# Kernel optimization log

Measured on AMD Instinct MI355X. Metric: run time of the kernel, lower is better.

Reference implementation:

```python
import jax, jax.numpy as jnp
import numpy as np

B, H, W = 32, 512, 512

def _sample(img, sx, sy):
    """Bilinear sample img [C,H,W] at source coords sx,sy [H,W]; zeros padding (align_corners=True pixel coords)."""
    C, Hh, Ww = img.shape
    x0 = jnp.floor(sx); y0 = jnp.floor(sy)
    wx = sx - x0; wy = sy - y0
    def gat(xf, yf):
        xi = jnp.clip(xf, 0, Ww - 1).astype(jnp.int32)
        yi = jnp.clip(yf, 0, Hh - 1).astype(jnp.int32)
        valid = ((xf >= 0) & (xf <= Ww - 1) & (yf >= 0) & (yf <= Hh - 1)).astype(img.dtype)
        return img[:, yi, xi] * valid
    return (gat(x0, y0) * (1 - wx) * (1 - wy) + gat(x0 + 1, y0) * wx * (1 - wy)
            + gat(x0, y0 + 1) * (1 - wx) * wy + gat(x0 + 1, y0 + 1) * wx * wy)

def _grid(Hh, Ww, dtype):
    ys, xs = jnp.meshgrid(jnp.arange(Hh, dtype=dtype), jnp.arange(Ww, dtype=dtype), indexing='ij')
    return xs, ys

def _rotate_one(img, angle_deg):
    C, Hh, Ww = img.shape
    th = angle_deg * (jnp.pi / 180.0)
    c, s = jnp.cos(th), jnp.sin(th)
    cx, cy = (Ww - 1) / 2.0, (Hh - 1) / 2.0
    xs, ys = _grid(Hh, Ww, img.dtype)
    dx, dy = xs - cx, ys - cy
    return _sample(img, c * dx + s * dy + cx, -s * dx + c * dy + cy)

def _affine_one(img, tx, ty, sc):
    C, Hh, Ww = img.shape
    cx, cy = (Ww - 1) / 2.0, (Hh - 1) / 2.0
    xs, ys = _grid(Hh, Ww, img.dtype)
    return _sample(img, (xs - cx - tx) / sc + cx, (ys - cy - ty) / sc + cy)

def _rgb_to_hsv(img):
    r, g, b = img[:, 0], img[:, 1], img[:, 2]
    maxc = jnp.maximum(jnp.maximum(r, g), b)
    minc = jnp.minimum(jnp.minimum(r, g), b)
    delta = maxc - minc
    eps = 1e-8
    s = delta / (maxc + eps)
    dd = delta + eps
    rc, gc, bc = (maxc - r) / dd, (maxc - g) / dd, (maxc - b) / dd
    h = jnp.where(maxc == r, bc - gc, jnp.where(maxc == g, 2.0 + rc - bc, 4.0 + gc - rc))
    return (h / 6.0) % 1.0, s, maxc

def _hsv_to_rgb(h, s, v):
    i = jnp.floor(h * 6.0)
    f = h * 6.0 - i
    p, q, t = v * (1 - s), v * (1 - f * s), v * (1 - (1 - f) * s)
    i = i.astype(jnp.int32) % 6
    conds = [i == k for k in range(6)]
    r = jnp.select(conds, [v, q, p, p, t, v])
    g = jnp.select(conds, [t, v, v, q, p, p])
    b = jnp.select(conds, [p, p, t, v, v, q])
    return jnp.stack([r, g, b], axis=1)

def _color_jitter(img, bf, cf, sf, hf):
    bf, cf, sf = (x[:, None, None, None] for x in (bf, cf, sf))
    img = jnp.clip(img * bf, 0.0, 1.0)
    gray = (0.299 * img[:, 0] + 0.587 * img[:, 1] + 0.114 * img[:, 2])[:, None]
    mean = gray.mean(axis=(2, 3), keepdims=True)
    img = jnp.clip(cf * img + (1 - cf) * mean, 0.0, 1.0)
    gray = (0.299 * img[:, 0] + 0.587 * img[:, 1] + 0.114 * img[:, 2])[:, None]
    img = jnp.clip(sf * img + (1 - sf) * gray, 0.0, 1.0)
    h, s, v = _rgb_to_hsv(img)
    h = (h + hf[:, None, None]) % 1.0
    return jnp.clip(_hsv_to_rgb(h, s, v), 0.0, 1.0)

def _forward(imgs, masks, hflip_mask, vflip_mask, angles, translate, scale, brightness, contrast, saturation, hue):
    hm = (hflip_mask > 0)[:, None, None, None]
    vm = (vflip_mask > 0)[:, None, None, None]
    imgs = jnp.where(hm, imgs[..., ::-1], imgs)
    masks = jnp.where(hm, masks[..., ::-1], masks)
    imgs = jnp.where(vm, imgs[..., ::-1, :], imgs)
    masks = jnp.where(vm, masks[..., ::-1, :], masks)
    rot = jax.vmap(_rotate_one)
    imgs = rot(imgs, angles)
    masks = rot(masks, angles)
    tx = translate[:, 0] * W
    ty = translate[:, 1] * H
    aff = jax.vmap(_affine_one)
    imgs = aff(imgs, tx, ty, scale)
    masks = aff(masks, tx, ty, scale)
    imgs = _color_jitter(imgs, brightness, contrast, saturation, hue)
    return imgs, masks

def setup_inputs():
    key = jax.random.key(0)
    ks = jax.random.split(key, 11)
    return {
        "imgs": jax.random.uniform(ks[0], (B, 3, H, W), jnp.float32),
        "masks": (jax.random.uniform(ks[1], (B, 1, H, W)) > 0.5).astype(jnp.float32),
        "hflip_mask": jax.random.randint(ks[2], (B,), 0, 2, jnp.int32),
        "vflip_mask": jax.random.randint(ks[3], (B,), 0, 2, jnp.int32),
        "angles": (jax.random.uniform(ks[4], (B,)) - 0.5) * 180.0,
        "translate": (jax.random.uniform(ks[5], (B, 2)) - 0.5) * 0.2,
        "scale": 0.9 + jax.random.uniform(ks[6], (B,)) * 0.2,
        "brightness": 0.8 + jax.random.uniform(ks[7], (B,)) * 0.4,
        "contrast": 0.8 + jax.random.uniform(ks[8], (B,)) * 0.4,
        "saturation": 0.8 + jax.random.uniform(ks[9], (B,)) * 0.4,
        "hue": (jax.random.uniform(ks[10], (B,)) - 0.5) * 0.2,
    }

def reference(imgs, masks, hflip_mask, vflip_mask, angles, translate, scale, brightness, contrast, saturation, hue):
    return _forward(imgs, masks, hflip_mask, vflip_mask, angles, translate, scale, brightness, contrast, saturation, hue)
```

## Files before the change

### kernel.cpp

```cpp
#include <hip/hip_runtime.h>
#include <hip/hip_fp16.h>
#include <math.h>

#define Wd 512
#define Hd 512
#define Bd 32
#define PLANE (Hd * Wd)

#define WIN 48
#define WSTR 50
#define NPR1 (WIN * (WIN / 2))

#define AWIN 40
#define ASTR 42
#define NPR2 (AWIN * (AWIN / 2))

__device__ __forceinline__ float clip01(float x) { return fminf(fmaxf(x, 0.f), 1.f); }

__device__ __forceinline__ unsigned pack2h(float a, float b) {
    __half2 h = __floats2half2_rn(a, b);
    return *(unsigned*)&h;
}
__device__ __forceinline__ float2 unp2h(unsigned u) {
    return __half22float2(*(__half2*)&u);
}

__global__ __launch_bounds__(256) void k_rotate(const float* __restrict__ imgs,
                                                const float* __restrict__ masks,
                                                const int* __restrict__ hflip,
                                                const int* __restrict__ vflip,
                                                const float* __restrict__ angles,
                                                uint2* __restrict__ rot)
{
    __shared__ uint2 cells[WIN * WSTR];

    const int hw = blockIdx.x;
    const int lt = (hw & 7) * 1024 + (hw >> 3);
    const int b   = lt >> 8;
    const int t   = lt & 255;
    const int bx  = (t & 15) * 32;
    const int by  = (t >> 4) * 32;

    const int tx = threadIdx.x, ty = threadIdx.y;
    const int tid = ty * 32 + tx;

    const float cx = (Wd - 1) * 0.5f, cy = (Hd - 1) * 0.5f;
    const float th = angles[b] * 0.017453292519943295f;
    const float c = cosf(th), s = sinf(th);
    const bool hf = hflip[b] > 0, vf = vflip[b] > 0;

    const float xs0 = (float)bx - cx, xs1 = (float)(bx + 31) - cx;
    const float ys0 = (float)by - cy, ys1 = (float)(by + 31) - cy;
    float a0 = c * xs0 + s * ys0 + cx, a1 = c * xs1 + s * ys0 + cx;
    float a2 = c * xs0 + s * ys1 + cx, a3 = c * xs1 + s * ys1 + cx;
    float b0 = -s * xs0 + c * ys0 + cy, b1 = -s * xs1 + c * ys0 + cy;
    float b2 = -s * xs0 + c * ys1 + cy, b3 = -s * xs1 + c * ys1 + cy;
    float mnx = fminf(fminf(a0, a1), fminf(a2, a3));
    float mxx = fmaxf(fmaxf(a0, a1), fmaxf(a2, a3));
    float mny = fminf(fminf(b0, b1), fminf(b2, b3));
    float mxy = fmaxf(fmaxf(b0, b1), fmaxf(b2, b3));
    const int ox0 = ((int)floorf(hf ? (511.f - mxx) : mnx) - 1) & ~1;
    const int oy0 = (int)floorf(vf ? (511.f - mxy) : mny) - 1;

    const float* ib = imgs + (size_t)b * 3 * PLANE;
    const float* mb = masks + (size_t)b * PLANE;

    #pragma unroll
    for (int it = 0; it < 5; ++it) {
        int slot = tid + it * 256;
        if (it < 4 || slot < NPR1) {
            int row = slot / (WIN / 2);
            int pc  = slot - row * (WIN / 2);
            int gy = min(max(oy0 + row, 0), Hd - 1);
            int gx = min(max(ox0 + 2 * pc, 0), Wd - 2) & ~1;
            int gi = gy * Wd + gx;
            float2 r2 = *(const float2*)(ib + gi);
            float2 g2 = *(const float2*)(ib + gi + PLANE);
            float2 b2v = *(const float2*)(ib + gi + 2 * PLANE);
            float2 m2 = *(const float2*)(mb + gi);
            uint4 w;
            w.x = pack2h(r2.x, g2.x);
            w.y = pack2h(b2v.x, m2.x);
            w.z = pack2h(r2.y, g2.y);
            w.w = pack2h(b2v.y, m2.y);
            *(uint4*)&cells[row * WSTR + 2 * pc] = w;
        }
    }
    __syncthreads();

    #pragma unroll
    for (int k = 0; k < 4; ++k) {
        const int x = bx + tx, y = by + ty + k * 8;
        float dx = (float)x - cx, dy = (float)y - cy;
        float sx = c * dx + s * dy + cx;
        float sy = -s * dx + c * dy + cy;
        if (hf) sx = 511.f - sx;
        if (vf) sy = 511.f - sy;

        float sxl = sx - (float)ox0, syl = sy - (float)oy0;
        float x0f = floorf(sxl), y0f = floorf(syl);
        float wx = sxl - x0f, wy = syl - y0f;
        int xi = min(max((int)x0f, 0), WIN - 2);
        int yi = min(max((int)y0f, 0), WIN - 2);

        float fx0 = (float)ox0 + x0f, fy0 = (float)oy0 + y0f;
        float vx0 = (fx0 >= 0.f && fx0 <= 511.f) ? 1.f : 0.f;
        float vx1 = (fx0 >= -1.f && fx0 <= 510.f) ? 1.f : 0.f;
        float vy0 = (fy0 >= 0.f && fy0 <= 511.f) ? 1.f : 0.f;
        float vy1 = (fy0 >= -1.f && fy0 <= 510.f) ? 1.f : 0.f;
        float w00 = (1.f - wx) * (1.f - wy) * vx0 * vy0;
        float w10 = wx * (1.f - wy) * vx1 * vy0;
        float w01 = (1.f - wx) * wy * vx0 * vy1;
        float w11 = wx * wy * vx1 * vy1;

        int base = yi * WSTR + xi;
        uint2 c00 = cells[base],        c10 = cells[base + 1];
        uint2 c01 = cells[base + WSTR], c11 = cells[base + WSTR + 1];

        float2 rg00 = unp2h(c00.x), bm00 = unp2h(c00.y);
        float2 rg10 = unp2h(c10.x), bm10 = unp2h(c10.y);
        float2 rg01 = unp2h(c01.x), bm01 = unp2h(c01.y);
        float2 rg11 = unp2h(c11.x), bm11 = unp2h(c11.y);

        float r  = w00 * rg00.x + w10 * rg10.x + w01 * rg01.x + w11 * rg11.x;
        float g  = w00 * rg00.y + w10 * rg10.y + w01 * rg01.y + w11 * rg11.y;
        float bl = w00 * bm00.x + w10 * bm10.x + w01 * bm01.x + w11 * bm11.x;
        float m  = w00 * bm00.y + w10 * bm10.y + w01 * bm01.y + w11 * bm11.y;

        rot[(size_t)b * PLANE + (size_t)y * Wd + x] =
            make_uint2(pack2h(r, g), pack2h(bl, m));
    }
}

__global__ __launch_bounds__(256) void k_affine(const uint2* __restrict__ rot,
                                                const float* __restrict__ translate,
                                                const float* __restrict__ scale,
                                                const float* __restrict__ brightness,
                                                unsigned short* __restrict__ pre,
                                                float* __restrict__ omasks,
                                                float* __restrict__ partials)
{
    __shared__ uint2 tile[AWIN * ASTR];

    const int hw = blockIdx.x;
    const int lt = (hw & 7) * 1024 + (hw >> 3);
    const int b   = lt >> 8;
    const int t   = lt & 255;
    const int bx  = (t & 15) * 32;
    const int by  = (t >> 4) * 32;

    const int tx2 = threadIdx.x;
    const int ty  = threadIdx.y;
    const int tid = ty * 16 + tx2;

    const float cx = (Wd - 1) * 0.5f, cy = (Hd - 1) * 0.5f;
    const float txf = translate[2 * b] * (float)Wd;
    const float tyf = translate[2 * b + 1] * (float)Hd;
    const float sc = scale[b];
    const float bf = brightness[b];

    float ax0 = ((float)bx - cx - txf) / sc + cx;
    float ax1 = ((float)(bx + 31) - cx - txf) / sc + cx;
    float ay0 = ((float)by - cy - tyf) / sc + cy;
    float ay1 = ((float)(by + 31) - cy - tyf) / sc + cy;
    const int rx0 = (((int)floorf(fminf(ax0, ax1)) - 1) & ~1);
    const int ry0 = (int)floorf(fminf(ay0, ay1)) - 1;

    const uint2* sb = rot + (size_t)b * PLANE;

    #pragma unroll
    for (int it = 0; it < 4; ++it) {
        int slot = tid + it * 256;
        if (it < 3 || slot < NPR2) {
            int row = slot / (AWIN / 2);
            int pc  = slot - row * (AWIN / 2);
            int gy = min(max(ry0 + row, 0), Hd - 1);
            int gx = min(max(rx0 + 2 * pc, 0), Wd - 2) & ~1;
            uint4 v = *(const uint4*)(sb + gy * Wd + gx);
            *(uint4*)&tile[row * ASTR + 2 * pc] = v;
        }
    }
    __syncthreads();

    float grays = 0.f;
    #pragma unroll
    for (int j = 0; j < 2; ++j) {
        float rr[2], gg[2], bb[2], mm[2];
        const int y = by + ty + 16 * j;
        #pragma unroll
        for (int k = 0; k < 2; ++k) {
            int x = bx + 2 * tx2 + k;
            float sx = ((float)x - cx - txf) / sc + cx;
            float sy = ((float)y - cy - tyf) / sc + cy;
            float sxl = sx - (float)rx0, syl = sy - (float)ry0;
            float x0f = floorf(sxl), y0f = floorf(syl);
            float wx = sxl - x0f, wy = syl - y0f;
            int xi = min(max((int)x0f, 0), AWIN - 2);
            int yi = min(max((int)y0f, 0), AWIN - 2);

            float fx0 = (float)rx0 + x0f, fy0 = (float)ry0 + y0f;
            float vx0 = (fx0 >= 0.f && fx0 <= 511.f) ? 1.f : 0.f;
            float vx1 = (fx0 >= -1.f && fx0 <= 510.f) ? 1.f : 0.f;
            float vy0 = (fy0 >= 0.f && fy0 <= 511.f) ? 1.f : 0.f;
            float vy1 = (fy0 >= -1.f && fy0 <= 510.f) ? 1.f : 0.f;
            float w00 = (1.f - wx) * (1.f - wy) * vx0 * vy0;
            float w10 = wx * (1.f - wy) * vx1 * vy0;
            float w01 = (1.f - wx) * wy * vx0 * vy1;
            float w11 = wx * wy * vx1 * vy1;

            int base = yi * ASTR + xi;
            uint2 c00 = tile[base],        c10 = tile[base + 1];
            uint2 c01 = tile[base + ASTR], c11 = tile[base + ASTR + 1];
            float2 rg00 = unp2h(c00.x), bm00 = unp2h(c00.y);
            float2 rg10 = unp2h(c10.x), bm10 = unp2h(c10.y);
            float2 rg01 = unp2h(c01.x), bm01 = unp2h(c01.y);
            float2 rg11 = unp2h(c11.x), bm11 = unp2h(c11.y);

            float r  = w00 * rg00.x + w10 * rg10.x + w01 * rg01.x + w11 * rg11.x;
            float g  = w00 * rg00.y + w10 * rg10.y + w01 * rg01.y + w11 * rg11.y;
            float b2 = w00 * bm00.x + w10 * bm10.x + w01 * bm01.x + w11 * bm11.x;
            float m  = w00 * bm00.y + w10 * bm10.y + w01 * bm01.y + w11 * bm11.y;

            r = clip01(r * bf);
            g = clip01(g * bf);
            b2 = clip01(b2 * bf);
            rr[k] = r; gg[k] = g; bb[k] = b2; mm[k] = m;
            grays += 0.299f * r + 0.587f * g + 0.114f * b2;
        }
        size_t pix = (size_t)y * Wd + bx + 2 * tx2;
        unsigned short* pb = pre + (size_t)b * 3 * PLANE;
        *(unsigned*)(pb + pix)             = pack2h(rr[0], rr[1]);
        *(unsigned*)(pb + PLANE + pix)     = pack2h(gg[0], gg[1]);
        *(unsigned*)(pb + 2 * PLANE + pix) = pack2h(bb[0], bb[1]);
        *(float2*)(omasks + (size_t)b * PLANE + pix) = make_float2(mm[0], mm[1]);
    }

    __syncthreads();
    float* sred = (float*)tile;
    sred[tid] = grays;
    __syncthreads();
    for (int off = 128; off > 0; off >>= 1) {
        if (tid < off) sred[tid] += sred[tid + off];
        __syncthreads();
    }
    if (tid == 0)
        partials[(size_t)b * 256 + t] = sred[0];
}

__global__ __launch_bounds__(256) void k_mean(const float* __restrict__ partials,
                                              float* __restrict__ means)
{
    int b = blockIdx.x;
    int t = threadIdx.x;
    float s = partials[(size_t)b * 256 + t];
    __shared__ float sr[256];
    sr[t] = s;
    __syncthreads();
    for (int off = 128; off > 0; off >>= 1) {
        if (t < off) sr[t] += sr[t + off];
        __syncthreads();
    }
    if (t == 0) means[b] = sr[0] * (1.f / (float)PLANE);
}

__device__ __forceinline__ void jit1(float& r, float& g, float& bl,
                                     float mean, float cf, float sf, float hsh)
{
    r  = clip01(cf * r + (1.f - cf) * mean);
    g  = clip01(cf * g + (1.f - cf) * mean);
    bl = clip01(cf * bl + (1.f - cf) * mean);

    float gray = 0.299f * r + 0.587f * g + 0.114f * bl;
    r  = clip01(sf * r + (1.f - sf) * gray);
    g  = clip01(sf * g + (1.f - sf) * gray);
    bl = clip01(sf * bl + (1.f - sf) * gray);

    float maxc = fmaxf(fmaxf(r, g), bl);
    float minc = fminf(fminf(r, g), bl);
    float delta = maxc - minc;
    float sgm = delta / (maxc + 1e-8f);
    float dd = delta + 1e-8f;
    float rc = (maxc - r) / dd;
    float gc = (maxc - g) / dd;
    float bc = (maxc - bl) / dd;
    float h6 = (maxc == r) ? (bc - gc) : ((maxc == g) ? (2.f + rc - bc) : (4.f + gc - rc));
    float h = h6 * (1.f / 6.f);
    h = h - floorf(h);
    h = h + hsh;
    h = h - floorf(h);

    float hi = floorf(h * 6.f);
    float f = h * 6.f - hi;
    float v = maxc;
    float p = v * (1.f - sgm);
    float q = v * (1.f - f * sgm);
    float t = v * (1.f - (1.f - f) * sgm);
    int i = ((int)hi) % 6;
    if (i < 0) i += 6;
    float ro, go, bo;
    switch (i) {
        case 0: ro = v; go = t; bo = p; break;
        case 1: ro = q; go = v; bo = p; break;
        case 2: ro = p; go = v; bo = t; break;
        case 3: ro = p; go = q; bo = v; break;
        case 4: ro = t; go = p; bo = v; break;
        default: ro = v; go = p; bo = q; break;
    }
    r = clip01(ro); g = clip01(go); bl = clip01(bo);
}

__global__ __launch_bounds__(256) void k_jitter(const unsigned short* __restrict__ pre,
                                                const float* __restrict__ means,
                                                const float* __restrict__ contrast,
                                                const float* __restrict__ saturation,
                                                const float* __restrict__ hue,
                                                float* __restrict__ oimgs)
{
    int b = blockIdx.y;
    size_t i4 = (size_t)blockIdx.x * 256 + threadIdx.x;
    const unsigned short* pb = pre + (size_t)b * 3 * PLANE;

    uint2 ur = *(const uint2*)(pb + i4 * 4);
    uint2 ug = *(const uint2*)(pb + PLANE + i4 * 4);
    uint2 ub = *(const uint2*)(pb + 2 * PLANE + i4 * 4);

    float2 r01 = unp2h(ur.x), r23 = unp2h(ur.y);
    float2 g01 = unp2h(ug.x), g23 = unp2h(ug.y);
    float2 b01 = unp2h(ub.x), b23 = unp2h(ub.y);

    float4 R  = make_float4(r01.x, r01.y, r23.x, r23.y);
    float4 G  = make_float4(g01.x, g01.y, g23.x, g23.y);
    float4 Bv = make_float4(b01.x, b01.y, b23.x, b23.y);

    float mean = means[b];
    float cf = contrast[b], sf = saturation[b], hsh = hue[b];

    jit1(R.x, G.x, Bv.x, mean, cf, sf, hsh);
    jit1(R.y, G.y, Bv.y, mean, cf, sf, hsh);
    jit1(R.z, G.z, Bv.z, mean, cf, sf, hsh);
    jit1(R.w, G.w, Bv.w, mean, cf, sf, hsh);

    size_t po = (size_t)b * 3 * PLANE + i4 * 4;
    *(float4*)(oimgs + po)             = R;
    *(float4*)(oimgs + po + PLANE)     = G;
    *(float4*)(oimgs + po + 2 * PLANE) = Bv;
}

extern "C" void kernel_launch(void* const* d_in, const int* in_sizes, int n_in,
                              void* d_out, int out_size, void* d_ws, size_t ws_size,
                              hipStream_t stream)
{
    const float* imgs       = (const float*)d_in[0];
    const float* masks      = (const float*)d_in[1];
    const int*   hflip      = (const int*)d_in[2];
    const int*   vflip      = (const int*)d_in[3];
    const float* angles     = (const float*)d_in[4];
    const float* translate  = (const float*)d_in[5];
    const float* scale      = (const float*)d_in[6];
    const float* brightness = (const float*)d_in[7];
    const float* contrast   = (const float*)d_in[8];
    const float* saturation = (const float*)d_in[9];
    const float* hue        = (const float*)d_in[10];

    float* oimgs  = (float*)d_out;
    float* omasks = oimgs + (size_t)Bd * 3 * PLANE;

    uint2* rot          = (uint2*)d_ws;
    unsigned short* pre = (unsigned short*)(rot + (size_t)Bd * PLANE);
    float* partials     = (float*)(pre + (size_t)3 * Bd * PLANE);
    float* means        = partials + (size_t)Bd * 256;

    dim3 blk1(32, 8);
    dim3 grd1(Bd * 16 * 16);
    k_rotate<<<grd1, blk1, 0, stream>>>(imgs, masks, hflip, vflip, angles, rot);

    dim3 blk2(16, 16);
    dim3 grd2(Bd * 16 * 16);
    k_affine<<<grd2, blk2, 0, stream>>>(rot, translate, scale, brightness,
                                        pre, omasks, partials);

    k_mean<<<Bd, 256, 0, stream>>>(partials, means);

    dim3 grd3(PLANE / 4 / 256, Bd);
    k_jitter<<<grd3, 256, 0, stream>>>(pre, means, contrast, saturation, hue, oimgs);
}
```

Baseline: 118.0 us.

## Widen rotate tile loads to float4 and fold mean reduction into jitter

The rotate kernel now stages its source window with float4 loads over a 4-aligned, slightly wider window, which needs fewer load iterations per thread. The separate per-image mean kernel is removed. Each jitter block instead reduces the 256 partial sums itself in shared memory and uses a swizzled block index. This removes one launch and its serialization, at the cost of redundant small reductions in every jitter block.

New measurement: 116.1 us. About the same (-1.6%).

```diff
diff --git a/kernel.cpp b/kernel.cpp
--- a/kernel.cpp
+++ b/kernel.cpp
@@ -7,9 +7,10 @@
 #define Bd 32
 #define PLANE (Hd * Wd)
 
-#define WIN 48
-#define WSTR 50
-#define NPR1 (WIN * (WIN / 2))
+#define WINR 48
+#define WINC 52
+#define WSTR 54
+#define NQ1 (WINR * (WINC / 4))
 
 #define AWIN 40
 #define ASTR 42
@@ -32,7 +33,7 @@
                                                 const float* __restrict__ angles,
                                                 uint2* __restrict__ rot)
 {
-    __shared__ uint2 cells[WIN * WSTR];
+    __shared__ uint2 cells[WINR * WSTR];
 
     const int hw = blockIdx.x;
     const int lt = (hw & 7) * 1024 + (hw >> 3);
@@ -59,31 +60,33 @@
     float mxx = fmaxf(fmaxf(a0, a1), fmaxf(a2, a3));
     float mny = fminf(fminf(b0, b1), fminf(b2, b3));
     float mxy = fmaxf(fmaxf(b0, b1), fmaxf(b2, b3));
-    const int ox0 = ((int)floorf(hf ? (511.f - mxx) : mnx) - 1) & ~1;
+    const int ox0 = ((int)floorf(hf ? (511.f - mxx) : mnx) - 1) & ~3;
     const int oy0 = (int)floorf(vf ? (511.f - mxy) : mny) - 1;
 
     const float* ib = imgs + (size_t)b * 3 * PLANE;
     const float* mb = masks + (size_t)b * PLANE;
 
     #pragma unroll
-    for (int it = 0; it < 5; ++it) {
+    for (int it = 0; it < 3; ++it) {
         int slot = tid + it * 256;
-        if (it < 4 || slot < NPR1) {
-            int row = slot / (WIN / 2);
-            int pc  = slot - row * (WIN / 2);
+        if (it < 2 || slot < NQ1) {
+            int row = slot / (WINC / 4);
+            int qc  = slot - row * (WINC / 4);
             int gy = min(max(oy0 + row, 0), Hd - 1);
-            int gx = min(max(ox0 + 2 * pc, 0), Wd - 2) & ~1;
+            int gx = min(max(ox0 + 4 * qc, 0), Wd - 4);
             int gi = gy * Wd + gx;
-            float2 r2 = *(const float2*)(ib + gi);
-            float2 g2 = *(const float2*)(ib + gi + PLANE);
-            float2 b2v = *(const float2*)(ib + gi + 2 * PLANE);
-            float2 m2 = *(const float2*)(mb + gi);
-            uint4 w;
-            w.x = pack2h(r2.x, g2.x);
-            w.y = pack2h(b2v.x, m2.x);
-            w.z = pack2h(r2.y, g2.y);
-            w.w = pack2h(b2v.y, m2.y);
-            *(uint4*)&cells[row * WSTR + 2 * pc] = w;
+            float4 r4 = *(const float4*)(ib + gi);
+            float4 g4 = *(const float4*)(ib + gi + PLANE);
+            float4 b4 = *(const float4*)(ib + gi + 2 * PLANE);
+            float4 m4 = *(const float4*)(mb + gi);
+            uint4 w0, w1;
+            w0.x = pack2h(r4.x, g4.x); w0.y = pack2h(b4.x, m4.x);
+            w0.z = pack2h(r4.y, g4.y); w0.w = pack2h(b4.y, m4.y);
+            w1.x = pack2h(r4.z, g4.z); w1.y = pack2h(b4.z, m4.z);
+            w1.z = pack2h(r4.w, g4.w); w1.w = pack2h(b4.w, m4.w);
+            uint2* cp = &cells[row * WSTR + 4 * qc];
+            *(uint4*)cp       = w0;
+            *(uint4*)(cp + 2) = w1;
         }
     }
     __syncthreads();
@@ -100,8 +103,8 @@
         float sxl = sx - (float)ox0, syl = sy - (float)oy0;
         float x0f = floorf(sxl), y0f = floorf(syl);
         float wx = sxl - x0f, wy = syl - y0f;
-        int xi = min(max((int)x0f, 0), WIN - 2);
-        int yi = min(max((int)y0f, 0), WIN - 2);
+        int xi = min(max((int)x0f, 0), WINC - 2);
+        int yi = min(max((int)y0f, 0), WINR - 2);
 
         float fx0 = (float)ox0 + x0f, fy0 = (float)oy0 + y0f;
         float vx0 = (fx0 >= 0.f && fx0 <= 511.f) ? 1.f : 0.f;
@@ -245,22 +248,6 @@
     }
     if (tid == 0)
         partials[(size_t)b * 256 + t] = sred[0];
-}
-
-__global__ __launch_bounds__(256) void k_mean(const float* __restrict__ partials,
-                                              float* __restrict__ means)
-{
-    int b = blockIdx.x;
-    int t = threadIdx.x;
-    float s = partials[(size_t)b * 256 + t];
-    __shared__ float sr[256];
-    sr[t] = s;
-    __syncthreads();
-    for (int off = 128; off > 0; off >>= 1) {
-        if (t < off) sr[t] += sr[t + off];
-        __syncthreads();
-    }
-    if (t == 0) means[b] = sr[0] * (1.f / (float)PLANE);
 }
 
 __device__ __forceinline__ void jit1(float& r, float& g, float& bl,
@@ -310,14 +297,28 @@
 }
 
 __global__ __launch_bounds__(256) void k_jitter(const unsigned short* __restrict__ pre,
-                                                const float* __restrict__ means,
+                                                const float* __restrict__ partials,
                                                 const float* __restrict__ contrast,
                                                 const float* __restrict__ saturation,
                                                 const float* __restrict__ hue,
                                                 float* __restrict__ oimgs)
 {
-    int b = blockIdx.y;
-    size_t i4 = (size_t)blockIdx.x * 256 + threadIdx.x;
+    const int hw = blockIdx.x;
+    const int lt = (hw & 7) * 1024 + (hw >> 3);
+    const int b   = lt >> 8;
+    const int blk = lt & 255;
+    const int tid = threadIdx.x;
+
+    __shared__ float sr[256];
+    sr[tid] = partials[(size_t)b * 256 + tid];
+    __syncthreads();
+    for (int off = 128; off > 0; off >>= 1) {
+        if (tid < off) sr[tid] += sr[tid + off];
+        __syncthreads();
+    }
+    float mean = sr[0] * (1.f / (float)PLANE);
+
+    size_t i4 = (size_t)blk * 256 + tid;
     const unsigned short* pb = pre + (size_t)b * 3 * PLANE;
 
     uint2 ur = *(const uint2*)(pb + i4 * 4);
@@ -332,7 +333,6 @@
     float4 G  = make_float4(g01.x, g01.y, g23.x, g23.y);
     float4 Bv = make_float4(b01.x, b01.y, b23.x, b23.y);
 
-    float mean = means[b];
     float cf = contrast[b], sf = saturation[b], hsh = hue[b];
 
     jit1(R.x, G.x, Bv.x, mean, cf, sf, hsh);
@@ -368,7 +368,6 @@
     uint2* rot          = (uint2*)d_ws;
     unsigned short* pre = (unsigned short*)(rot + (size_t)Bd * PLANE);
     float* partials     = (float*)(pre + (size_t)3 * Bd * PLANE);
-    float* means        = partials + (size_t)Bd * 256;
 
     dim3 blk1(32, 8);
     dim3 grd1(Bd * 16 * 16);
@@ -379,8 +378,6 @@
     k_affine<<<grd2, blk2, 0, stream>>>(rot, translate, scale, brightness,
                                         pre, omasks, partials);
 
-    k_mean<<<Bd, 256, 0, stream>>>(partials, means);
-
-    dim3 grd3(PLANE / 4 / 256, Bd);
-    k_jitter<<<grd3, 256, 0, stream>>>(pre, means, contrast, saturation, hue, oimgs);
-}
+    dim3 grd3(Bd * 256);
+    k_jitter<<<grd3, 256, 0, stream>>>(pre, partials, contrast, saturation, hue, oimgs);
+}
```
